# Performance work log

Measured on AMD Instinct MI355X. Metric: run time of the kernel, lower is better.

Reference implementation:

```python
import jax, jax.numpy as jnp
import numpy as np

N_NODES = 100000
N_EDGES = 1600000
D = 128
HID = 256  # min(2*D, 256)
D_OUT = 128
BN_EPS = 1e-5


def setup_inputs() -> dict:
    key = jax.random.key(0)
    ks = jax.random.split(key, 16)
    s = 0.05
    inp = {
        "x": jax.random.normal(ks[0], (N_NODES, D), dtype=jnp.float32),
        "edges": jax.random.randint(ks[1], (2, N_EDGES), 0, N_NODES, dtype=jnp.int32),
        # affine_before_rnn: Linear(D, D)
        "W_aff": jax.random.normal(ks[2], (D, D), dtype=jnp.float32) * s,
        "b_aff": jnp.zeros((D,), dtype=jnp.float32),
        # GRUCell(D, D)
        "W_ih": jax.random.normal(ks[3], (3 * D, D), dtype=jnp.float32) * s,
        "b_ih": jnp.zeros((3 * D,), dtype=jnp.float32),
        "W_hh": jax.random.normal(ks[4], (3 * D, D), dtype=jnp.float32) * s,
        "b_hh": jnp.zeros((3 * D,), dtype=jnp.float32),
        # merge_layer: Linear(2*D, D)
        "W_merge": jax.random.normal(ks[5], (D, 2 * D), dtype=jnp.float32) * s,
        "b_merge": jnp.zeros((D,), dtype=jnp.float32),
        # learnable self-connection weight
        "eps": jnp.asarray(1.0, dtype=jnp.float32),
        # backbone: Linear(D, HID) -> relu -> Linear(HID, D_OUT) -> relu -> BatchNorm1d
        "W1": jax.random.normal(ks[6], (HID, D), dtype=jnp.float32) * s,
        "b1": jnp.zeros((HID,), dtype=jnp.float32),
        "W2": jax.random.normal(ks[7], (D_OUT, HID), dtype=jnp.float32) * s,
        "b2": jnp.zeros((D_OUT,), dtype=jnp.float32),
        "gamma": jnp.ones((D_OUT,), dtype=jnp.float32),
        "beta": jnp.zeros((D_OUT,), dtype=jnp.float32),
    }
    return inp


def reference(x, edges, W_aff, b_aff, W_ih, b_ih, W_hh, b_hh,
              W_merge, b_merge, eps, W1, b1, W2, b2, gamma, beta):
    src, dst = edges[0], edges[1]
    n = x.shape[0]

    # ---- aggregation 1: 'sum' -> scatter-sum of neighbor features ----
    agg_sum = jax.ops.segment_sum(x[src], dst, num_segments=n)  # (N, D)

    # ---- aggregation 2: 'rnn-max' -> affine, scatter-max, GRUCell ----
    xi = x @ W_aff.T + b_aff
    agg_max = jax.ops.segment_max(xi[src], dst, num_segments=n)  # (N, D)
    agg_max = jnp.where(jnp.isfinite(agg_max), agg_max, 0.0)  # empty segments -> 0

    # GRUCell: input = aggregated neighbors, hidden = original node features
    gi = agg_max @ W_ih.T + b_ih  # (N, 3D)
    gh = x @ W_hh.T + b_hh        # (N, 3D)
    ir, iz, inn = jnp.split(gi, 3, axis=1)
    hr, hz, hn = jnp.split(gh, 3, axis=1)
    r = jax.nn.sigmoid(ir + hr)
    z = jax.nn.sigmoid(iz + hz)
    ncand = jnp.tanh(inn + r * hn)
    rnn_out = (1.0 - z) * ncand + z * x  # (N, D)

    # ---- merge ('cat') ----
    h = jnp.concatenate([agg_sum, rnn_out], axis=1) @ W_merge.T + b_merge  # (N, D)

    # ---- learnable self-connection ----
    h = h + eps * x

    # ---- backbone: dense -> relu -> dense -> relu -> batchnorm1d (train mode) ----
    h = jax.nn.relu(h @ W1.T + b1)
    h = jax.nn.relu(h @ W2.T + b2)
    mean = jnp.mean(h, axis=0)
    var = jnp.mean(jnp.square(h - mean), axis=0)  # biased batch variance
    out = gamma * (h - mean) * jax.lax.rsqrt(var + BN_EPS) + beta
    return out
```

## Files before the change

kernel.cpp:

```cpp
#include <hip/hip_runtime.h>
#include <hip/hip_bf16.h>
#include <math.h>

using bf16 = __hip_bfloat16;
typedef __attribute__((ext_vector_type(8))) short bf16x8;
typedef __attribute__((ext_vector_type(4))) float f32x4;

__device__ __forceinline__ float b2f(unsigned short u) {
  return __uint_as_float(((unsigned)u) << 16);
}
__device__ __forceinline__ unsigned short f2b(float f) {
  bf16 h = __float2bfloat16(f);
  return *reinterpret_cast<unsigned short*>(&h);
}
__device__ __forceinline__ ushort4 f2b4(float4 v) {
  return make_ushort4(f2b(v.x), f2b(v.y), f2b(v.z), f2b(v.w));
}

__global__ __launch_bounds__(256) void mgemm_k(
    const unsigned short* __restrict__ A, int lda, const float* __restrict__ W,
    const float* __restrict__ bias, unsigned short* __restrict__ Cb, int ldc,
    int N, int M, int K) {
  constexpr int LDA = 72;
  __shared__ unsigned short As[128 * LDA];
  __shared__ unsigned short Ws[128 * LDA];

  const int tid = threadIdx.x;
  const int lane = tid & 63;
  const int wave = tid >> 6;
  const int row0 = blockIdx.y * 128;
  const int m0 = blockIdx.x * 128;
  const int rowhalf = (wave & 1) * 64;
  const int colhalf = (wave >> 1) * 64;
  const int l15 = lane & 15;
  const int quad = lane >> 4;

  f32x4 acc[4][4] = {};

  for (int kc = 0; kc < K; kc += 64) {
#pragma unroll
    for (int i = 0; i < 4; i++) {
      int idx = tid + i * 256;
      int r = idx >> 3;
      int k8 = (idx & 7) * 8;
      int row = row0 + r;
      ushort4 u0 = make_ushort4(0, 0, 0, 0), u1 = u0;
      if (row < N) {
        const unsigned short* s = A + (size_t)row * lda + kc + k8;
        u0 = *(const ushort4*)s;
        u1 = *(const ushort4*)(s + 4);
      }
      *(ushort4*)&As[r * LDA + k8] = u0;
      *(ushort4*)&As[r * LDA + k8 + 4] = u1;
    }
#pragma unroll
    for (int i = 0; i < 8; i++) {
      int idx = tid + i * 256;
      int r = idx >> 4;
      int k4 = idx & 15;
      float4 v = *(const float4*)(W + (size_t)(m0 + r) * K + kc + k4 * 4);
      *(ushort4*)&Ws[r * LDA + k4 * 4] = f2b4(v);
    }
    __syncthreads();
#pragma unroll
    for (int ks = 0; ks < 2; ks++) {
      const int ko = ks * 32 + quad * 8;
      bf16x8 af[4], wf[4];
#pragma unroll
      for (int ri = 0; ri < 4; ri++)
        af[ri] = *(const bf16x8*)&As[(rowhalf + ri * 16 + l15) * LDA + ko];
#pragma unroll
      for (int ci = 0; ci < 4; ci++)
        wf[ci] = *(const bf16x8*)&Ws[(colhalf + ci * 16 + l15) * LDA + ko];
#pragma unroll
      for (int ri = 0; ri < 4; ri++)
#pragma unroll
        for (int ci = 0; ci < 4; ci++)
          acc[ri][ci] = __builtin_amdgcn_mfma_f32_16x16x32_bf16(
              af[ri], wf[ci], acc[ri][ci], 0, 0, 0);
    }
    __syncthreads();
  }
#pragma unroll
  for (int ci = 0; ci < 4; ci++) {
    const int col = m0 + colhalf + ci * 16 + l15;
    const float bv = bias[col];
#pragma unroll
    for (int ri = 0; ri < 4; ri++) {
      const int rbase = row0 + rowhalf + ri * 16 + quad * 4;
#pragma unroll
      for (int r = 0; r < 4; r++) {
        int row = rbase + r;
        if (row >= N) continue;
        Cb[(size_t)row * ldc + col] = f2b(acc[ri][ci][r] + bv);
      }
    }
  }
}

__global__ __launch_bounds__(256) void grurnn_k(
    const unsigned short* __restrict__ aggm,
    const unsigned short* __restrict__ xcat,
    const unsigned short* __restrict__ Wbig,
    const float* __restrict__ bias_big, unsigned short* __restrict__ Bcat,
    int N) {
  constexpr int LDA = 264;
  __shared__ unsigned short As[32 * LDA];

  const int tid = threadIdx.x;
  const int lane = tid & 63;
  const int wave = tid >> 6;
  const int l15 = lane & 15;
  const int quad = lane >> 4;
  const int row0 = blockIdx.x * 32;

  {
    int r = tid >> 3;
    int k32 = (tid & 7) * 32;
    int row = row0 + r;
    uint4 u[4] = {};
    if (row < N) {
      const unsigned short* s = (k32 < 128)
                                    ? aggm + (size_t)row * 128 + k32
                                    : xcat + (size_t)row * 256 + (k32 - 128);
#pragma unroll
      for (int i = 0; i < 4; i++) u[i] = *(const uint4*)(s + i * 8);
    }
#pragma unroll
    for (int i = 0; i < 4; i++)
      *(uint4*)&As[r * LDA + k32 + i * 8] = u[i];
  }
  __syncthreads();

  f32x4 acc[2][8] = {};
#pragma unroll
  for (int ks = 0; ks < 8; ks++) {
    const int ko = ks * 32 + quad * 8;
    bf16x8 af0 = *(const bf16x8*)&As[l15 * LDA + ko];
    bf16x8 af1 = *(const bf16x8*)&As[(16 + l15) * LDA + ko];
#pragma unroll
    for (int ci = 0; ci < 8; ci++) {
      int m = wave * 128 + ci * 16 + l15;
      bf16x8 wf = *(const bf16x8*)&Wbig[(size_t)m * 256 + ko];
      acc[0][ci] = __builtin_amdgcn_mfma_f32_16x16x32_bf16(af0, wf,
                                                           acc[0][ci], 0, 0, 0);
      acc[1][ci] = __builtin_amdgcn_mfma_f32_16x16x32_bf16(af1, wf,
                                                           acc[1][ci], 0, 0, 0);
    }
  }
  unsigned short outv[2][2][4];
#pragma unroll
  for (int fi = 0; fi < 2; fi++) {
    const int f = wave * 32 + fi * 16 + l15;
    const float br = bias_big[f];
    const float bz = bias_big[128 + f];
    const float bi = bias_big[256 + f];
    const float bh = bias_big[384 + f];
#pragma unroll
    for (int ri = 0; ri < 2; ri++) {
#pragma unroll
      for (int r = 0; r < 4; r++) {
        int rl = ri * 16 + quad * 4 + r;
        float rg = 1.f / (1.f + __expf(-(acc[ri][4 * fi + 0][r] + br)));
        float zg = 1.f / (1.f + __expf(-(acc[ri][4 * fi + 1][r] + bz)));
        float a =
            acc[ri][4 * fi + 2][r] + bi + rg * (acc[ri][4 * fi + 3][r] + bh);
        float t = 1.f - 2.f / (__expf(2.f * fabsf(a)) + 1.f);
        float nc = copysignf(t, a);
        float xv = b2f(As[rl * LDA + 128 + f]);
        outv[fi][ri][r] = f2b((1.f - zg) * nc + zg * xv);
      }
    }
  }
  __syncthreads();
#pragma unroll
  for (int fi = 0; fi < 2; fi++) {
    const int f = wave * 32 + fi * 16 + l15;
#pragma unroll
    for (int ri = 0; ri < 2; ri++)
#pragma unroll
      for (int r = 0; r < 4; r++)
        As[(ri * 16 + quad * 4 + r) * LDA + f] = outv[fi][ri][r];
  }
  __syncthreads();
#pragma unroll
  for (int j = 0; j < 2; j++) {
    int idx = tid + j * 256;
    int rl = idx >> 4;
    int c8 = (idx & 15) * 8;
    int row = row0 + rl;
    if (row < N)
      *(uint4*)&Bcat[(size_t)row * 256 + 128 + c8] =
          *(const uint4*)&As[rl * LDA + c8];
  }
}

__global__ __launch_bounds__(256) void backbone_k(
    const unsigned short* __restrict__ Bcat,
    const unsigned short* __restrict__ xcat,
    const unsigned short* __restrict__ Wmb, const float* __restrict__ bm,
    const unsigned short* __restrict__ W1b, const float* __restrict__ b1,
    const unsigned short* __restrict__ W2b, const float* __restrict__ b2,
    const float* __restrict__ epsp, float* __restrict__ out,
    float* __restrict__ stats, int N) {
  constexpr int LDH = 136;
  __shared__ unsigned short Hp[64 * LDH];
  __shared__ unsigned short Hd[64 * LDH];
  __shared__ float sbn[128], qbn[128];

  const int tid = threadIdx.x;
  const int lane = tid & 63;
  const int wave = tid >> 6;
  const int l15 = lane & 15;
  const int quad = lane >> 4;
  const int row0 = blockIdx.x * 64;
  if (tid < 128) {
    sbn[tid] = 0.f;
    qbn[tid] = 0.f;
  }
  const float ep = epsp[0];

  {
    f32x4 acc[4][2] = {};
#pragma unroll
    for (int ks = 0; ks < 8; ks++) {
      const int ko = ks * 32 + quad * 8;
      bf16x8 af[4];
#pragma unroll
      for (int ri = 0; ri < 4; ri++)
        af[ri] =
            *(const bf16x8*)&Bcat[(size_t)(row0 + ri * 16 + l15) * 256 + ko];
#pragma unroll
      for (int ci = 0; ci < 2; ci++) {
        bf16x8 wf =
            *(const bf16x8*)&Wmb[(size_t)(wave * 32 + ci * 16 + l15) * 256 + ko];
#pragma unroll
        for (int ri = 0; ri < 4; ri++)
          acc[ri][ci] = __builtin_amdgcn_mfma_f32_16x16x32_bf16(
              af[ri], wf, acc[ri][ci], 0, 0, 0);
      }
    }
#pragma unroll
    for (int ci = 0; ci < 2; ci++) {
      int c = wave * 32 + ci * 16 + l15;
      float bv = bm[c];
#pragma unroll
      for (int ri = 0; ri < 4; ri++) {
#pragma unroll
        for (int r = 0; r < 4; r++) {
          int lr = ri * 16 + quad * 4 + r;
          int row = row0 + lr;
          float v = acc[ri][ci][r] + bv;
          if (row < N) v += ep * b2f(xcat[(size_t)row * 256 + c]);
          Hp[lr * LDH + c] = f2b(v);
        }
      }
    }
  }
  __syncthreads();

  f32x4 acc3[4][2] = {};
#pragma unroll
  for (int hh = 0; hh < 2; hh++) {
    f32x4 acc2[4][2] = {};
#pragma unroll
    for (int ks = 0; ks < 4; ks++) {
      const int ko = ks * 32 + quad * 8;
      bf16x8 af[4];
#pragma unroll
      for (int ri = 0; ri < 4; ri++)
        af[ri] = *(const bf16x8*)&Hp[(ri * 16 + l15) * LDH + ko];
#pragma unroll
      for (int ci = 0; ci < 2; ci++) {
        bf16x8 wf = *(const bf16x8*)&W1b[(size_t)(hh * 128 + wave * 32 +
                                                  ci * 16 + l15) *
                                             128 +
                                         ko];
#pragma unroll
        for (int ri = 0; ri < 4; ri++)
          acc2[ri][ci] = __builtin_amdgcn_mfma_f32_16x16x32_bf16(
              af[ri], wf, acc2[ri][ci], 0, 0, 0);
      }
    }
    __syncthreads();
#pragma unroll
    for (int ci = 0; ci < 2; ci++) {
      int c = wave * 32 + ci * 16 + l15;
      float bv = b1[hh * 128 + c];
#pragma unroll
      for (int ri = 0; ri < 4; ri++) {
#pragma unroll
        for (int r = 0; r < 4; r++) {
          int lr = ri * 16 + quad * 4 + r;
          Hd[lr * LDH + c] = f2b(fmaxf(acc2[ri][ci][r] + bv, 0.f));
        }
      }
    }
    __syncthreads();
#pragma unroll
    for (int ks = 0; ks < 4; ks++) {
      const int ko = ks * 32 + quad * 8;
      bf16x8 af[4];
#pragma unroll
      for (int ri = 0; ri < 4; ri++)
        af[ri] = *(const bf16x8*)&Hd[(ri * 16 + l15) * LDH + ko];
#pragma unroll
      for (int ci = 0; ci < 2; ci++) {
        bf16x8 wf = *(const bf16x8*)&W2b[(size_t)(wave * 32 + ci * 16 + l15) *
                                             256 +
                                         hh * 128 + ko];
#pragma unroll
        for (int ri = 0; ri < 4; ri++)
          acc3[ri][ci] = __builtin_amdgcn_mfma_f32_16x16x32_bf16(
              af[ri], wf, acc3[ri][ci], 0, 0, 0);
      }
    }
  }
#pragma unroll
  for (int ci = 0; ci < 2; ci++) {
    int c = wave * 32 + ci * 16 + l15;
    float bv = b2[c];
    float s = 0.f, q = 0.f;
#pragma unroll
    for (int ri = 0; ri < 4; ri++) {
#pragma unroll
      for (int r = 0; r < 4; r++) {
        int lr = ri * 16 + quad * 4 + r;
        int row = row0 + lr;
        if (row >= N) continue;
        float v = fmaxf(acc3[ri][ci][r] + bv, 0.f);
        out[(size_t)row * 128 + c] = v;
        s += v;
        q += v * v;
      }
    }
    atomicAdd(&sbn[c], s);
    atomicAdd(&qbn[c], q);
  }
  __syncthreads();
  if (tid < 128) {
    atomicAdd(&stats[tid], sbn[tid]);
    atomicAdd(&stats[128 + tid], qbn[tid]);
  }
}

__global__ __launch_bounds__(256) void prep_k(
    const float* __restrict__ W_ih, const float* __restrict__ b_ih,
    const float* __restrict__ W_hh, const float* __restrict__ b_hh,
    const float* __restrict__ Wm, const float* __restrict__ W1,
    const float* __restrict__ W2, unsigned short* __restrict__ Wbig,
    unsigned short* __restrict__ Wmb, unsigned short* __restrict__ W1b,
    unsigned short* __restrict__ W2b, float* __restrict__ bias_big,
    float* __restrict__ stats, int* __restrict__ deg, int N) {
  int idx = blockIdx.x * 256 + threadIdx.x;
  if (idx < N) deg[idx] = 0;
  if (idx < 32768) {
    int mp = idx >> 6;
    int k4 = (idx & 63) * 4;
    int w = mp >> 7, ci = (mp >> 4) & 7, l15 = mp & 15;
    int g = ci & 3, fi = ci >> 2;
    int f = w * 32 + fi * 16 + l15;
    const float* src = nullptr;
    int koff = 0;
    if (g <= 1) {
      int m = g * 128 + f;
      if (k4 < 128) { src = W_ih + (size_t)m * 128; koff = k4; }
      else          { src = W_hh + (size_t)m * 128; koff = k4 - 128; }
    } else if (g == 2) {
      if (k4 < 128) { src = W_ih + (size_t)(256 + f) * 128; koff = k4; }
    } else {
      if (k4 >= 128) { src = W_hh + (size_t)(256 + f) * 128; koff = k4 - 128; }
    }
    ushort4 o = make_ushort4(0, 0, 0, 0);
    if (src) o = f2b4(*(const float4*)(src + koff));
    *(ushort4*)&Wbig[(size_t)mp * 256 + k4] = o;
  }
  if (idx < 8192) {
    int m = idx >> 6;
    int k4 = (idx & 63) * 4;
    *(ushort4*)&Wmb[(size_t)m * 256 + k4] =
        f2b4(*(const float4*)(Wm + (size_t)m * 256 + k4));
    *(ushort4*)&W2b[(size_t)m * 256 + k4] =
        f2b4(*(const float4*)(W2 + (size_t)m * 256 + k4));
    int m2 = idx >> 5;
    int k42 = (idx & 31) * 4;
    *(ushort4*)&W1b[(size_t)m2 * 128 + k42] =
        f2b4(*(const float4*)(W1 + (size_t)m2 * 128 + k42));
  }
  if (blockIdx.x == 0) {
    int t = threadIdx.x;
    stats[t] = 0.f;
#pragma unroll
    for (int h = 0; h < 2; h++) {
      int mm = t + h * 256;
      float b;
      if (mm < 256) b = b_ih[mm] + b_hh[mm];
      else if (mm < 384) b = b_ih[mm];
      else b = b_hh[mm - 128];
      bias_big[mm] = b;
    }
  }
}

__global__ __launch_bounds__(256) void cvthist_k(
    const int* __restrict__ edges, int* __restrict__ deg, int E,
    const float* __restrict__ x, unsigned short* __restrict__ xcat,
    int ngroups, int eblk) {
  if ((int)blockIdx.x < eblk) {
    int e = blockIdx.x * 256 + threadIdx.x;
    if (e < E) atomicAdd(&deg[edges[(size_t)E + e]], 1);
  } else {
    int g = (blockIdx.x - eblk) * 256 + threadIdx.x;
    if (g >= ngroups) return;
    int n = g >> 5;
    int j = (g & 31) * 4;
    float4 v = *(const float4*)&x[(size_t)n * 128 + j];
    *(ushort4*)&xcat[(size_t)n * 256 + j] = f2b4(v);
  }
}

__global__ __launch_bounds__(256) void scan1_k(const int* __restrict__ deg,
                                               int* __restrict__ off,
                                               int* __restrict__ bsums, int N) {
  __shared__ int s[256];
  int t = threadIdx.x;
  int i = blockIdx.x * 256 + t;
  int v = (i < N) ? deg[i] : 0;
  s[t] = v;
  __syncthreads();
#pragma unroll
  for (int d = 1; d < 256; d <<= 1) {
    int u = (t >= d) ? s[t - d] : 0;
    __syncthreads();
    s[t] += u;
    __syncthreads();
  }
  if (i < N) off[i] = s[t] - v;
  if (t == 255) bsums[blockIdx.x] = s[255];
}

__global__ __launch_bounds__(512) void scan2_k(int* __restrict__ bsums,
                                               int nb) {
  __shared__ int s[512];
  int t = threadIdx.x;
  int v = (t < nb) ? bsums[t] : 0;
  s[t] = v;
  __syncthreads();
#pragma unroll
  for (int d = 1; d < 512; d <<= 1) {
    int u = (t >= d) ? s[t - d] : 0;
    __syncthreads();
    s[t] += u;
    __syncthreads();
  }
  if (t < nb) bsums[t] = s[t] - v;
}

__global__ __launch_bounds__(256) void scan3_k(int* __restrict__ off,
                                               const int* __restrict__ bsums,
                                               int* __restrict__ binoff,
                                               int* __restrict__ bincur,
                                               int N, int E, int NB) {
  int i = blockIdx.x * 256 + threadIdx.x;
  if (i < N) {
    int o = off[i] + bsums[blockIdx.x];
    off[i] = o;
    if ((i & 511) == 0) {
      binoff[i >> 9] = o;
      bincur[i >> 9] = o;
    }
  }
  if (i == 0) {
    off[N] = E;
    binoff[NB] = E;
  }
}

__global__ __launch_bounds__(256) void edgepart_k(const int* __restrict__ edges,
                                                  int* __restrict__ bincur,
                                                  int* __restrict__ part,
                                                  int E, int NB) {
  __shared__ int cnt[256];
  const int tid = threadIdx.x;
  if (tid < NB) cnt[tid] = 0;
  __syncthreads();
  int sv[16], dv[16];
  const int e0 = blockIdx.x * 4096;
#pragma unroll
  for (int i = 0; i < 16; i++) {
    int e = e0 + i * 256 + tid;
    int s = 0, d = -1;
    if (e < E) {
      s = edges[e];
      d = edges[(size_t)E + e];
    }
    sv[i] = s;
    dv[i] = d;
    if (d >= 0) atomicAdd(&cnt[d >> 9], 1);
  }
  __syncthreads();
  if (tid < NB) {
    int c = cnt[tid];
    int base = c ? atomicAdd(&bincur[tid], c) : 0;
    cnt[tid] = base;
  }
  __syncthreads();
#pragma unroll
  for (int i = 0; i < 16; i++) {
    int d = dv[i];
    if (d < 0) continue;
    int p = atomicAdd(&cnt[d >> 9], 1);
    part[p] = (sv[i] << 9) | (d & 511);
  }
}

__global__ __launch_bounds__(1024) void fill2_k(const int* __restrict__ off,
                                                const int* __restrict__ binoff,
                                                const int* __restrict__ part,
                                                int* __restrict__ bucket,
                                                int N) {
  __shared__ int scur[512];
  const int b = blockIdx.x;
  const int n0 = b << 9;
  const int tid = threadIdx.x;
  if (tid < 512) {
    int node = n0 + tid;
    scur[tid] = (node < N) ? off[node] : 0;
  }
  __syncthreads();
  const int j0 = binoff[b];
  const int j1 = binoff[b + 1];
  for (int j = j0 + tid; j < j1; j += 1024) {
    int p = part[j];
    int pos = atomicAdd(&scur[p & 511], 1);
    bucket[pos] = p >> 9;
  }
}

__global__ __launch_bounds__(256) void gather_k(
    const int* __restrict__ off, const int* __restrict__ bucket,
    const unsigned short* __restrict__ xcat, unsigned short* __restrict__ aggm,
    unsigned short* __restrict__ Bcat, int N) {
  int node = blockIdx.x * 4 + (threadIdx.x >> 6);
  if (node >= N) return;
  const int lane = threadIdx.x & 63;
  const int half = lane >> 5;
  const int f = (lane & 31) * 4;
  const int j0 = off[node], jend = off[node + 1];
  float s0 = 0.f, s1 = 0.f, s2 = 0.f, s3 = 0.f;
  float m0 = -INFINITY, m1 = -INFINITY, m2 = -INFINITY, m3 = -INFINITY;
  int jj = j0 + half;
  int p0 = (jj < jend) ? bucket[jj] : 0;
  int p1 = (jj + 2 < jend) ? bucket[jj + 2] : 0;
  for (; jj < jend; jj += 2) {
    int src = p0;
    p0 = p1;
    p1 = (jj + 4 < jend) ? bucket[jj + 4] : 0;
    ushort4 a = *(const ushort4*)(xcat + (size_t)src * 256 + f);
    ushort4 b = *(const ushort4*)(xcat + (size_t)src * 256 + 128 + f);
    s0 += b2f(a.x);
    s1 += b2f(a.y);
    s2 += b2f(a.z);
    s3 += b2f(a.w);
    m0 = fmaxf(m0, b2f(b.x));
    m1 = fmaxf(m1, b2f(b.y));
    m2 = fmaxf(m2, b2f(b.z));
    m3 = fmaxf(m3, b2f(b.w));
  }
  s0 += __shfl_xor(s0, 32);
  s1 += __shfl_xor(s1, 32);
  s2 += __shfl_xor(s2, 32);
  s3 += __shfl_xor(s3, 32);
  m0 = fmaxf(m0, __shfl_xor(m0, 32));
  m1 = fmaxf(m1, __shfl_xor(m1, 32));
  m2 = fmaxf(m2, __shfl_xor(m2, 32));
  m3 = fmaxf(m3, __shfl_xor(m3, 32));
  if (half == 0) {
    bool nz = jend > j0;
    ushort4 mv = nz ? make_ushort4(f2b(m0), f2b(m1), f2b(m2), f2b(m3))
                    : make_ushort4(0, 0, 0, 0);
    *(ushort4*)&aggm[(size_t)node * 128 + f] = mv;
    *(ushort4*)&Bcat[(size_t)node * 256 + f] =
        make_ushort4(f2b(s0), f2b(s1), f2b(s2), f2b(s3));
  }
}

__global__ __launch_bounds__(256) void bn_apply_k(
    float* __restrict__ out, const float* __restrict__ stats,
    const float* __restrict__ gamma, const float* __restrict__ beta,
    float invn, int nd4) {
  int g = blockIdx.x * 256 + threadIdx.x;
  if (g >= nd4) return;
  int d = (g & 31) * 4;
  float4 v = ((float4*)out)[g];
  float o[4] = {v.x, v.y, v.z, v.w};
#pragma unroll
  for (int i = 0; i < 4; i++) {
    float mean = stats[d + i] * invn;
    float var = fmaxf(stats[128 + d + i] * invn - mean * mean, 0.f);
    float sc = gamma[d + i] * rsqrtf(var + 1e-5f);
    o[i] = (o[i] - mean) * sc + beta[d + i];
  }
  ((float4*)out)[g] = make_float4(o[0], o[1], o[2], o[3]);
}

extern "C" void kernel_launch(void* const* d_in, const int* in_sizes, int n_in,
                              void* d_out, int out_size, void* d_ws,
                              size_t ws_size, hipStream_t stream) {
  (void)n_in;
  (void)out_size;
  (void)ws_size;
  const float* x = (const float*)d_in[0];
  const int* edges = (const int*)d_in[1];
  const float* W_aff = (const float*)d_in[2];
  const float* b_aff = (const float*)d_in[3];
  const float* W_ih = (const float*)d_in[4];
  const float* b_ih = (const float*)d_in[5];
  const float* W_hh = (const float*)d_in[6];
  const float* b_hh = (const float*)d_in[7];
  const float* W_merge = (const float*)d_in[8];
  const float* b_merge = (const float*)d_in[9];
  const float* epsp = (const float*)d_in[10];
  const float* W1 = (const float*)d_in[11];
  const float* b1 = (const float*)d_in[12];
  const float* W2 = (const float*)d_in[13];
  const float* b2 = (const float*)d_in[14];
  const float* gamma = (const float*)d_in[15];
  const float* beta = (const float*)d_in[16];

  const int N = in_sizes[0] / 128;
  const int E = in_sizes[1] / 2;
  const size_t nd = (size_t)N * 128;
  const int NB = (N + 511) >> 9;

  char* base = (char*)d_ws;
  unsigned short* xcat = (unsigned short*)base;
  unsigned short* Bcat = (unsigned short*)(base + (size_t)N * 512);
  unsigned short* aggm = (unsigned short*)(base + (size_t)N * 1024);
  unsigned short* Wbig = (unsigned short*)(base + (size_t)N * 1280);
  unsigned short* Wmb = Wbig + 512 * 256;
  unsigned short* W1b = Wmb + 128 * 256;
  unsigned short* W2b = W1b + 256 * 128;
  float* bias_big = (float*)(W2b + 128 * 256);
  float* stats = bias_big + 512;
  int* deg = (int*)(stats + 512);
  int* off = deg + N;
  int* binoff = off + N + 1;
  int* bincur = binoff + NB + 1;
  int* bucket = bincur + NB;
  int* bsums = bucket + E;
  float* out = (float*)d_out;
  int* part = (int*)d_out;

  const int ny = (N + 127) / 128;
  const int nblk = (N + 255) / 256;
  const int eblk = (E + 255) / 256;
  const int cvtblk = (int)((nd / 4 + 255) / 256);
  const int pgrid = nblk > 128 ? nblk : 128;
  dim3 blk(256);

  prep_k<<<pgrid, blk, 0, stream>>>(W_ih, b_ih, W_hh, b_hh, W_merge, W1, W2,
                                    Wbig, Wmb, W1b, W2b, bias_big, stats, deg,
                                    N);
  cvthist_k<<<eblk + cvtblk, blk, 0, stream>>>(edges, deg, E, x, xcat,
                                               (int)(nd / 4), eblk);
  scan1_k<<<nblk, blk, 0, stream>>>(deg, off, bsums, N);
  scan2_k<<<1, 512, 0, stream>>>(bsums, nblk);
  scan3_k<<<nblk, blk, 0, stream>>>(off, bsums, binoff, bincur, N, E, NB);
  edgepart_k<<<(E + 4095) / 4096, blk, 0, stream>>>(edges, bincur, part, E, NB);
  fill2_k<<<NB, dim3(1024), 0, stream>>>(off, binoff, part, bucket, N);

  mgemm_k<<<dim3(1, ny), blk, 0, stream>>>(xcat, 256, W_aff, b_aff, xcat + 128,
                                           256, N, 128, 128);
  gather_k<<<(N + 3) / 4, blk, 0, stream>>>(off, bucket, xcat, aggm, Bcat, N);
  grurnn_k<<<(N + 31) / 32, blk, 0, stream>>>(aggm, xcat, Wbig, bias_big,
                                              Bcat, N);
  backbone_k<<<(N + 63) / 64, blk, 0, stream>>>(Bcat, xcat, Wmb, b_merge, W1b,
                                                b1, W2b, b2, epsp, out, stats,
                                                N);
  bn_apply_k<<<(int)((nd / 4 + 255) / 256), blk, 0, stream>>>(
      out, stats, gamma, beta, 1.f / (float)N, (int)(nd / 4));
}
```

Baseline: 638.8 us.

## Fuse GRU cell kernel with merge/backbone MLP kernel

Merges the GRU gate kernel and the backbone kernel into one kernel over 32-row tiles. The GRU output and the sum-aggregation now stay in shared memory instead of going through a global Bcat buffer, which removes one launch and a full N x 256 bf16 write and read round trip. In exchange the backbone runs on 32-row tiles instead of 64, so weight fragments are reused less, and shared memory per block grows, which may lower occupancy.

```diff
diff --git a/kernel.cpp b/kernel.cpp
--- a/kernel.cpp
+++ b/kernel.cpp
@@ -98,14 +98,24 @@
   }
 }
 
-__global__ __launch_bounds__(256) void grurnn_k(
+__global__ __launch_bounds__(256) void grubb_k(
     const unsigned short* __restrict__ aggm,
     const unsigned short* __restrict__ xcat,
+    const unsigned short* __restrict__ aggs,
     const unsigned short* __restrict__ Wbig,
-    const float* __restrict__ bias_big, unsigned short* __restrict__ Bcat,
-    int N) {
+    const float* __restrict__ bias_big,
+    const unsigned short* __restrict__ Wmb, const float* __restrict__ bm,
+    const unsigned short* __restrict__ W1b, const float* __restrict__ b1,
+    const unsigned short* __restrict__ W2b, const float* __restrict__ b2,
+    const float* __restrict__ epsp, float* __restrict__ out,
+    float* __restrict__ stats, int N) {
   constexpr int LDA = 264;
+  constexpr int LDH = 136;
   __shared__ unsigned short As[32 * LDA];
+  __shared__ unsigned short Acat[32 * LDA];
+  __shared__ unsigned short Hp[32 * LDH];
+  __shared__ float sbn[128], qbn[128];
+  unsigned short* Hd = As;
 
   const int tid = threadIdx.x;
   const int lane = tid & 63;
@@ -113,131 +123,96 @@
   const int l15 = lane & 15;
   const int quad = lane >> 4;
   const int row0 = blockIdx.x * 32;
+  if (tid < 128) {
+    sbn[tid] = 0.f;
+    qbn[tid] = 0.f;
+  }
+  const float ep = epsp[0];
 
   {
     int r = tid >> 3;
     int k32 = (tid & 7) * 32;
     int row = row0 + r;
     uint4 u[4] = {};
+    uint4 v[2] = {};
     if (row < N) {
       const unsigned short* s = (k32 < 128)
                                     ? aggm + (size_t)row * 128 + k32
                                     : xcat + (size_t)row * 256 + (k32 - 128);
 #pragma unroll
       for (int i = 0; i < 4; i++) u[i] = *(const uint4*)(s + i * 8);
-    }
-#pragma unroll
-    for (int i = 0; i < 4; i++)
-      *(uint4*)&As[r * LDA + k32 + i * 8] = u[i];
-  }
-  __syncthreads();
-
-  f32x4 acc[2][8] = {};
-#pragma unroll
-  for (int ks = 0; ks < 8; ks++) {
-    const int ko = ks * 32 + quad * 8;
-    bf16x8 af0 = *(const bf16x8*)&As[l15 * LDA + ko];
-    bf16x8 af1 = *(const bf16x8*)&As[(16 + l15) * LDA + ko];
-#pragma unroll
-    for (int ci = 0; ci < 8; ci++) {
-      int m = wave * 128 + ci * 16 + l15;
-      bf16x8 wf = *(const bf16x8*)&Wbig[(size_t)m * 256 + ko];
-      acc[0][ci] = __builtin_amdgcn_mfma_f32_16x16x32_bf16(af0, wf,
-                                                           acc[0][ci], 0, 0, 0);
-      acc[1][ci] = __builtin_amdgcn_mfma_f32_16x16x32_bf16(af1, wf,
-                                                           acc[1][ci], 0, 0, 0);
-    }
-  }
-  unsigned short outv[2][2][4];
-#pragma unroll
-  for (int fi = 0; fi < 2; fi++) {
-    const int f = wave * 32 + fi * 16 + l15;
-    const float br = bias_big[f];
-    const float bz = bias_big[128 + f];
-    const float bi = bias_big[256 + f];
-    const float bh = bias_big[384 + f];
-#pragma unroll
-    for (int ri = 0; ri < 2; ri++) {
-#pragma unroll
-      for (int r = 0; r < 4; r++) {
-        int rl = ri * 16 + quad * 4 + r;
-        float rg = 1.f / (1.f + __expf(-(acc[ri][4 * fi + 0][r] + br)));
-        float zg = 1.f / (1.f + __expf(-(acc[ri][4 * fi + 1][r] + bz)));
-        float a =
-            acc[ri][4 * fi + 2][r] + bi + rg * (acc[ri][4 * fi + 3][r] + bh);
-        float t = 1.f - 2.f / (__expf(2.f * fabsf(a)) + 1.f);
-        float nc = copysignf(t, a);
-        float xv = b2f(As[rl * LDA + 128 + f]);
-        outv[fi][ri][r] = f2b((1.f - zg) * nc + zg * xv);
-      }
-    }
-  }
-  __syncthreads();
-#pragma unroll
-  for (int fi = 0; fi < 2; fi++) {
-    const int f = wave * 32 + fi * 16 + l15;
-#pragma unroll
-    for (int ri = 0; ri < 2; ri++)
-#pragma unroll
-      for (int r = 0; r < 4; r++)
-        As[(ri * 16 + quad * 4 + r) * LDA + f] = outv[fi][ri][r];
-  }
-  __syncthreads();
-#pragma unroll
-  for (int j = 0; j < 2; j++) {
-    int idx = tid + j * 256;
-    int rl = idx >> 4;
-    int c8 = (idx & 15) * 8;
-    int row = row0 + rl;
-    if (row < N)
-      *(uint4*)&Bcat[(size_t)row * 256 + 128 + c8] =
-          *(const uint4*)&As[rl * LDA + c8];
-  }
-}
-
-__global__ __launch_bounds__(256) void backbone_k(
-    const unsigned short* __restrict__ Bcat,
-    const unsigned short* __restrict__ xcat,
-    const unsigned short* __restrict__ Wmb, const float* __restrict__ bm,
-    const unsigned short* __restrict__ W1b, const float* __restrict__ b1,
-    const unsigned short* __restrict__ W2b, const float* __restrict__ b2,
-    const float* __restrict__ epsp, float* __restrict__ out,
-    float* __restrict__ stats, int N) {
-  constexpr int LDH = 136;
-  __shared__ unsigned short Hp[64 * LDH];
-  __shared__ unsigned short Hd[64 * LDH];
-  __shared__ float sbn[128], qbn[128];
-
-  const int tid = threadIdx.x;
-  const int lane = tid & 63;
-  const int wave = tid >> 6;
-  const int l15 = lane & 15;
-  const int quad = lane >> 4;
-  const int row0 = blockIdx.x * 64;
-  if (tid < 128) {
-    sbn[tid] = 0.f;
-    qbn[tid] = 0.f;
-  }
-  const float ep = epsp[0];
+      const unsigned short* s2 = aggs + (size_t)row * 128 + (tid & 7) * 16;
+      v[0] = *(const uint4*)s2;
+      v[1] = *(const uint4*)(s2 + 8);
+    }
+#pragma unroll
+    for (int i = 0; i < 4; i++) *(uint4*)&As[r * LDA + k32 + i * 8] = u[i];
+    int k16 = (tid & 7) * 16;
+    *(uint4*)&Acat[r * LDA + k16] = v[0];
+    *(uint4*)&Acat[r * LDA + k16 + 8] = v[1];
+  }
+  __syncthreads();
 
   {
-    f32x4 acc[4][2] = {};
+    f32x4 acc[2][8] = {};
 #pragma unroll
     for (int ks = 0; ks < 8; ks++) {
       const int ko = ks * 32 + quad * 8;
-      bf16x8 af[4];
-#pragma unroll
-      for (int ri = 0; ri < 4; ri++)
-        af[ri] =
-            *(const bf16x8*)&Bcat[(size_t)(row0 + ri * 16 + l15) * 256 + ko];
+      bf16x8 af0 = *(const bf16x8*)&As[l15 * LDA + ko];
+      bf16x8 af1 = *(const bf16x8*)&As[(16 + l15) * LDA + ko];
+#pragma unroll
+      for (int ci = 0; ci < 8; ci++) {
+        int m = wave * 128 + ci * 16 + l15;
+        bf16x8 wf = *(const bf16x8*)&Wbig[(size_t)m * 256 + ko];
+        acc[0][ci] = __builtin_amdgcn_mfma_f32_16x16x32_bf16(af0, wf,
+                                                             acc[0][ci], 0, 0, 0);
+        acc[1][ci] = __builtin_amdgcn_mfma_f32_16x16x32_bf16(af1, wf,
+                                                             acc[1][ci], 0, 0, 0);
+      }
+    }
+#pragma unroll
+    for (int fi = 0; fi < 2; fi++) {
+      const int f = wave * 32 + fi * 16 + l15;
+      const float br = bias_big[f];
+      const float bz = bias_big[128 + f];
+      const float bi = bias_big[256 + f];
+      const float bh = bias_big[384 + f];
+#pragma unroll
+      for (int ri = 0; ri < 2; ri++) {
+#pragma unroll
+        for (int r = 0; r < 4; r++) {
+          int rl = ri * 16 + quad * 4 + r;
+          float rg = 1.f / (1.f + __expf(-(acc[ri][4 * fi + 0][r] + br)));
+          float zg = 1.f / (1.f + __expf(-(acc[ri][4 * fi + 1][r] + bz)));
+          float a =
+              acc[ri][4 * fi + 2][r] + bi + rg * (acc[ri][4 * fi + 3][r] + bh);
+          float t = 1.f - 2.f / (__expf(2.f * fabsf(a)) + 1.f);
+          float nc = copysignf(t, a);
+          float xv = b2f(As[rl * LDA + 128 + f]);
+          Acat[rl * LDA + 128 + f] = f2b((1.f - zg) * nc + zg * xv);
+        }
+      }
+    }
+  }
+  __syncthreads();
+
+  {
+    f32x4 accm[2][2] = {};
+#pragma unroll
+    for (int ks = 0; ks < 8; ks++) {
+      const int ko = ks * 32 + quad * 8;
+      bf16x8 af[2];
+#pragma unroll
+      for (int ri = 0; ri < 2; ri++)
+        af[ri] = *(const bf16x8*)&Acat[(ri * 16 + l15) * LDA + ko];
 #pragma unroll
       for (int ci = 0; ci < 2; ci++) {
         bf16x8 wf =
             *(const bf16x8*)&Wmb[(size_t)(wave * 32 + ci * 16 + l15) * 256 + ko];
 #pragma unroll
-        for (int ri = 0; ri < 4; ri++)
-          acc[ri][ci] = __builtin_amdgcn_mfma_f32_16x16x32_bf16(
-              af[ri], wf, acc[ri][ci], 0, 0, 0);
+        for (int ri = 0; ri < 2; ri++)
+          accm[ri][ci] = __builtin_amdgcn_mfma_f32_16x16x32_bf16(
+              af[ri], wf, accm[ri][ci], 0, 0, 0);
       }
     }
 #pragma unroll
@@ -245,30 +220,28 @@
       int c = wave * 32 + ci * 16 + l15;
       float bv = bm[c];
 #pragma unroll
-      for (int ri = 0; ri < 4; ri++) {
+      for (int ri = 0; ri < 2; ri++) {
 #pragma unroll
         for (int r = 0; r < 4; r++) {
-          int lr = ri * 16 + quad * 4 + r;
-          int row = row0 + lr;
-          float v = acc[ri][ci][r] + bv;
-          if (row < N) v += ep * b2f(xcat[(size_t)row * 256 + c]);
-          Hp[lr * LDH + c] = f2b(v);
+          int rl = ri * 16 + quad * 4 + r;
+          float v = accm[ri][ci][r] + bv + ep * b2f(As[rl * LDA + 128 + c]);
+          Hp[rl * LDH + c] = f2b(v);
         }
       }
     }
   }
   __syncthreads();
 
-  f32x4 acc3[4][2] = {};
+  f32x4 acc3[2][2] = {};
 #pragma unroll
   for (int hh = 0; hh < 2; hh++) {
-    f32x4 acc2[4][2] = {};
+    f32x4 acc2[2][2] = {};
 #pragma unroll
     for (int ks = 0; ks < 4; ks++) {
       const int ko = ks * 32 + quad * 8;
-      bf16x8 af[4];
-#pragma unroll
-      for (int ri = 0; ri < 4; ri++)
+      bf16x8 af[2];
+#pragma unroll
+      for (int ri = 0; ri < 2; ri++)
         af[ri] = *(const bf16x8*)&Hp[(ri * 16 + l15) * LDH + ko];
 #pragma unroll
       for (int ci = 0; ci < 2; ci++) {
@@ -277,7 +250,7 @@
                                              128 +
                                          ko];
 #pragma unroll
-        for (int ri = 0; ri < 4; ri++)
+        for (int ri = 0; ri < 2; ri++)
           acc2[ri][ci] = __builtin_amdgcn_mfma_f32_16x16x32_bf16(
               af[ri], wf, acc2[ri][ci], 0, 0, 0);
       }
@@ -288,11 +261,11 @@
       int c = wave * 32 + ci * 16 + l15;
       float bv = b1[hh * 128 + c];
 #pragma unroll
-      for (int ri = 0; ri < 4; ri++) {
+      for (int ri = 0; ri < 2; ri++) {
 #pragma unroll
         for (int r = 0; r < 4; r++) {
-          int lr = ri * 16 + quad * 4 + r;
-          Hd[lr * LDH + c] = f2b(fmaxf(acc2[ri][ci][r] + bv, 0.f));
+          int rl = ri * 16 + quad * 4 + r;
+          Hd[rl * LDH + c] = f2b(fmaxf(acc2[ri][ci][r] + bv, 0.f));
         }
       }
     }
@@ -300,9 +273,9 @@
 #pragma unroll
     for (int ks = 0; ks < 4; ks++) {
       const int ko = ks * 32 + quad * 8;
-      bf16x8 af[4];
-#pragma unroll
-      for (int ri = 0; ri < 4; ri++)
+      bf16x8 af[2];
+#pragma unroll
+      for (int ri = 0; ri < 2; ri++)
         af[ri] = *(const bf16x8*)&Hd[(ri * 16 + l15) * LDH + ko];
 #pragma unroll
       for (int ci = 0; ci < 2; ci++) {
@@ -310,7 +283,7 @@
                                              256 +
                                          hh * 128 + ko];
 #pragma unroll
-        for (int ri = 0; ri < 4; ri++)
+        for (int ri = 0; ri < 2; ri++)
           acc3[ri][ci] = __builtin_amdgcn_mfma_f32_16x16x32_bf16(
               af[ri], wf, acc3[ri][ci], 0, 0, 0);
       }
@@ -322,11 +295,11 @@
     float bv = b2[c];
     float s = 0.f, q = 0.f;
 #pragma unroll
-    for (int ri = 0; ri < 4; ri++) {
+    for (int ri = 0; ri < 2; ri++) {
 #pragma unroll
       for (int r = 0; r < 4; r++) {
-        int lr = ri * 16 + quad * 4 + r;
-        int row = row0 + lr;
+        int rl = ri * 16 + quad * 4 + r;
+        int row = row0 + rl;
         if (row >= N) continue;
         float v = fmaxf(acc3[ri][ci][r] + bv, 0.f);
         out[(size_t)row * 128 + c] = v;
@@ -540,7 +513,7 @@
 __global__ __launch_bounds__(256) void gather_k(
     const int* __restrict__ off, const int* __restrict__ bucket,
     const unsigned short* __restrict__ xcat, unsigned short* __restrict__ aggm,
-    unsigned short* __restrict__ Bcat, int N) {
+    unsigned short* __restrict__ aggs, int N) {
   int node = blockIdx.x * 4 + (threadIdx.x >> 6);
   if (node >= N) return;
   const int lane = threadIdx.x & 63;
@@ -580,7 +553,7 @@
     ushort4 mv = nz ? make_ushort4(f2b(m0), f2b(m1), f2b(m2), f2b(m3))
                     : make_ushort4(0, 0, 0, 0);
     *(ushort4*)&aggm[(size_t)node * 128 + f] = mv;
-    *(ushort4*)&Bcat[(size_t)node * 256 + f] =
+    *(ushort4*)&aggs[(size_t)node * 128 + f] =
         make_ushort4(f2b(s0), f2b(s1), f2b(s2), f2b(s3));
   }
 }
@@ -635,7 +608,7 @@
 
   char* base = (char*)d_ws;
   unsigned short* xcat = (unsigned short*)base;
-  unsigned short* Bcat = (unsigned short*)(base + (size_t)N * 512);
+  unsigned short* aggs = (unsigned short*)(base + (size_t)N * 512);
   unsigned short* aggm = (unsigned short*)(base + (size_t)N * 1024);
   unsigned short* Wbig = (unsigned short*)(base + (size_t)N * 1280);
   unsigned short* Wmb = Wbig + 512 * 256;
@@ -672,12 +645,10 @@
 
   mgemm_k<<<dim3(1, ny), blk, 0, stream>>>(xcat, 256, W_aff, b_aff, xcat + 128,
                                            256, N, 128, 128);
-  gather_k<<<(N + 3) / 4, blk, 0, stream>>>(off, bucket, xcat, aggm, Bcat, N);
-  grurnn_k<<<(N + 31) / 32, blk, 0, stream>>>(aggm, xcat, Wbig, bias_big,
-                                              Bcat, N);
-  backbone_k<<<(N + 63) / 64, blk, 0, stream>>>(Bcat, xcat, Wmb, b_merge, W1b,
-                                                b1, W2b, b2, epsp, out, stats,
-                                                N);
+  gather_k<<<(N + 3) / 4, blk, 0, stream>>>(off, bucket, xcat, aggm, aggs, N);
+  grubb_k<<<(N + 31) / 32, blk, 0, stream>>>(aggm, xcat, aggs, Wbig, bias_big,
+                                             Wmb, b_merge, W1b, b1, W2b, b2,
+                                             epsp, out, stats, N);
   bn_apply_k<<<(int)((nd / 4 + 255) / 256), blk, 0, stream>>>(
       out, stats, gamma, beta, 1.f / (float)N, (int)(nd / 4));
 }
```

After: 620.4 us. -2.9%, faster.
